# Kernel tuning notes

Hardware: AMD Instinct MI355X
Metric: run time of the kernel (lower is better)

The kernel has to match this reference:

```python
import jax, jax.numpy as jnp
import numpy as np

B, T, IN = 4096, 64, 3
D, H, NB = 128, 4, 2
DH = D // H  # 32
EPS = 1e-5


def layer_norm(x, g, b):
    mu = x.mean(-1, keepdims=True)
    v = x.var(-1, keepdims=True)
    return (x - mu) / jnp.sqrt(v + EPS) * g + b


def group_norm(x, g, b):
    # headwise GroupNorm over the last dim split into H groups of DH
    xr = x.reshape(x.shape[:-1] + (H, DH))
    mu = xr.mean(-1, keepdims=True)
    v = xr.var(-1, keepdims=True)
    xn = ((xr - mu) / jnp.sqrt(v + EPS)).reshape(x.shape)
    return xn * g + b


def slstm(xg, R):
    # xg: [B,T,4,D] input-driven gate preactivations (i,f,z,o)
    # R : [4,H,DH,DH] block-diagonal (per-head) recurrent kernels per gate
    Bb = xg.shape[0]

    def step(carry, g):
        h, c, n, m = carry  # each [B,D]
        r = jnp.einsum('bhd,ghde->bghe', h.reshape(Bb, H, DH), R).reshape(Bb, 4, D)
        g = g + r
        it, ft, zt, ot = g[:, 0], g[:, 1], g[:, 2], g[:, 3]
        m_new = jnp.maximum(ft + m, it)          # stabilizer state
        i = jnp.exp(it - m_new)                  # stabilized exp input gate
        f = jnp.exp(ft + m - m_new)              # stabilized exp forget gate
        c_new = f * c + i * jnp.tanh(zt)
        n_new = f * n + i                        # normalizer state
        h_new = jax.nn.sigmoid(ot) * c_new / n_new
        return (h_new, c_new, n_new, m_new), h_new

    init = tuple(jnp.zeros((Bb, D), xg.dtype) for _ in range(4))
    _, hs = jax.lax.scan(step, init, jnp.swapaxes(xg, 0, 1))  # [T,B,D]
    return jnp.swapaxes(hs, 0, 1)


def setup_inputs() -> dict:
    key = jax.random.key(0)
    ks = jax.random.split(key, 12)
    s_in = 1.0 / np.sqrt(IN)
    s_d = 1.0 / np.sqrt(D)
    inp = {
        'x': jax.random.normal(ks[0], (B, T, IN), jnp.float32),
        'w_in': jax.random.normal(ks[1], (IN, D), jnp.float32) * s_in,
        'b_in': jnp.zeros((D,), jnp.float32),
        'ln1_g': jnp.ones((NB, D), jnp.float32),
        'ln1_b': jnp.zeros((NB, D), jnp.float32),
        'Wg': jax.random.normal(ks[2], (NB, D, 4 * D), jnp.float32) * s_d,
        'bg': jnp.zeros((NB, 4 * D), jnp.float32),
        'Rg': jax.random.normal(ks[3], (NB, 4, H, DH, DH), jnp.float32) / np.sqrt(DH),
        'gn_g': jnp.ones((NB, D), jnp.float32),
        'gn_b': jnp.zeros((NB, D), jnp.float32),
        'ln2_g': jnp.ones((NB, D), jnp.float32),
        'ln2_b': jnp.zeros((NB, D), jnp.float32),
        'W1': jax.random.normal(ks[4], (NB, D, D), jnp.float32) * s_d,
        'W2': jax.random.normal(ks[5], (NB, D, D), jnp.float32) * s_d,
        'lnf_g': jnp.ones((D,), jnp.float32),
        'lnf_b': jnp.zeros((D,), jnp.float32),
        'w_out': jax.random.normal(ks[6], (D, 1), jnp.float32) * s_d,
        'b_out': jnp.zeros((1,), jnp.float32),
    }
    return inp


def reference(x, w_in, b_in, ln1_g, ln1_b, Wg, bg, Rg, gn_g, gn_b,
              ln2_g, ln2_b, W1, W2, lnf_g, lnf_b, w_out, b_out):
    h = x @ w_in + b_in  # [B,T,D]
    for blk in range(NB):
        # sLSTM sub-block (pre-LN residual)
        xn = layer_norm(h, ln1_g[blk], ln1_b[blk])
        xg = (xn @ Wg[blk] + bg[blk]).reshape(h.shape[0], T, 4, D)
        hs = slstm(xg, Rg[blk])
        h = h + group_norm(hs, gn_g[blk], gn_b[blk])
        # FFN sub-block (pre-LN residual, proj_factor=1.0, gelu, no bias)
        yn = layer_norm(h, ln2_g[blk], ln2_b[blk])
        h = h + jax.nn.gelu(yn @ W1[blk]) @ W2[blk]
    h = layer_norm(h, lnf_g, lnf_b)  # post-blocks norm
    out = (h[:, -1, :] @ w_out + b_out)[:, 0]  # [B]
    return out
```

## Files before the change

### kernel.cpp

```cpp
#include <hip/hip_runtime.h>
#include <hip/hip_bf16.h>
#include <cstdint>
#include <cstddef>

#define EPS 1e-5f
#define BB 4096
#define TT 64
#define NBLK 2
#define MROWS (BB * TT)

typedef unsigned short ushort_t;
typedef __attribute__((ext_vector_type(8))) short short8;
typedef __attribute__((ext_vector_type(4))) float floatx4;

__device__ __forceinline__ ushort_t f2b(float f) {
    __hip_bfloat16 h = __float2bfloat16(f);
    return *reinterpret_cast<ushort_t*>(&h);
}
__device__ __forceinline__ float tanh_fast(float z) {
    return 1.f - 2.f / (__expf(2.f * z) + 1.f);
}
__device__ __forceinline__ void lds_barrier() {
    asm volatile("s_waitcnt lgkmcnt(0)\n\ts_barrier" ::: "memory");
}

template <int CTRL>
__device__ __forceinline__ float ror_add(float v) {
    int r = __builtin_amdgcn_update_dpp(
        0, __builtin_bit_cast(int, v), CTRL, 0xf, 0xf, false);
    return v + __builtin_bit_cast(float, r);
}
__device__ __forceinline__ float red16(float v) {
    v = ror_add<0x121>(v);
    v = ror_add<0x122>(v);
    v = ror_add<0x124>(v);
    v = ror_add<0x128>(v);
    return v;
}

__global__ __launch_bounds__(256) void k_cvtall(
    const float* __restrict__ Wg, const float* __restrict__ W1,
    const float* __restrict__ W2, ushort_t* __restrict__ Wgt,
    ushort_t* __restrict__ W1t, ushort_t* __restrict__ W2t) {
    int idx = blockIdx.x * 256 + threadIdx.x;
    if (idx < 2 * 512 * 128) {
        int blk = idx >> 16, r = idx & 65535;
        int n = r >> 7, k = r & 127;
        Wgt[idx] = f2b(Wg[(size_t)blk * 65536 + k * 512 + n]);
    } else if (idx < 2 * 512 * 128 + 2 * 128 * 128) {
        int i2 = idx - 2 * 512 * 128;
        int blk = i2 >> 14, r = i2 & 16383;
        int n = r >> 7, k = r & 127;
        W1t[i2] = f2b(W1[(size_t)blk * 16384 + k * 128 + n]);
    } else {
        int i2 = idx - (2 * 512 * 128 + 2 * 128 * 128);
        int blk = i2 >> 14, r = i2 & 16383;
        int n = r >> 7, k = r & 127;
        W2t[i2] = f2b(W2[(size_t)blk * 16384 + k * 128 + n]);
    }
}

template <bool EMBED, bool LASTONLY>
__global__ __launch_bounds__(512, 2) void k_gslstm(
    float* __restrict__ h, const float* __restrict__ x,
    const float* __restrict__ w_in, const float* __restrict__ b_in,
    const ushort_t* __restrict__ Wgt, const float* __restrict__ bg,
    const float* __restrict__ Rg,
    const float* __restrict__ ln1g, const float* __restrict__ ln1b,
    const float* __restrict__ gng, const float* __restrict__ gnb) {
    __shared__ float xg_ring[2][512][20];
    __shared__ float hin_ring[3][16][132];
    __shared__ ushort_t Afrag[2][16][136];
    __shared__ ushort_t tpose[4][16][40];

    const int tid = threadIdx.x;
    const int lane = tid & 63;
    const int wave = tid >> 6;
    const int q = lane >> 4;
    const int ml = lane & 15;
    const int b0 = blockIdx.x * 16;

    if (wave < 4) {
        const int p = wave;
        const int row = p * 4 + q;
        short8 WB[4][8];
#pragma unroll
        for (int ks = 0; ks < 4; ++ks)
#pragma unroll
            for (int s = 0; s < 8; ++s)
                WB[ks][s] = *(const short8*)(Wgt +
                    ((size_t)(p * 128 + s * 16 + ml) * 128 + ks * 32 + q * 8));
        float biasv[8];
#pragma unroll
        for (int s = 0; s < 8; ++s) biasv[s] = bg[p * 128 + s * 16 + ml];

        auto issue_in = [&](int tt, float4& A, float4& B) {
            const float4* hp =
                (const float4*)(h + ((size_t)(b0 + row) * TT + tt) * 128 + ml * 8);
            A = hp[0]; B = hp[1];
        };
        auto issue_x = [&](int tt, float& x0, float& x1, float& x2) {
            const float* xp = x + ((size_t)(b0 + row) * TT + tt) * 3;
            x0 = xp[0]; x1 = xp[1]; x2 = xp[2];
        };
        auto embed_v = [&](float x0, float x1, float x2, float* v) {
            float4 w00 = *(const float4*)(w_in + 0 * 128 + ml * 8);
            float4 w01 = *(const float4*)(w_in + 0 * 128 + ml * 8 + 4);
            float4 w10 = *(const float4*)(w_in + 1 * 128 + ml * 8);
            float4 w11 = *(const float4*)(w_in + 1 * 128 + ml * 8 + 4);
            float4 w20 = *(const float4*)(w_in + 2 * 128 + ml * 8);
            float4 w21 = *(const float4*)(w_in + 2 * 128 + ml * 8 + 4);
            float4 be0 = *(const float4*)(b_in + ml * 8);
            float4 be1 = *(const float4*)(b_in + ml * 8 + 4);
            const float w0[8] = {w00.x, w00.y, w00.z, w00.w, w01.x, w01.y, w01.z, w01.w};
            const float w1[8] = {w10.x, w10.y, w10.z, w10.w, w11.x, w11.y, w11.z, w11.w};
            const float w2[8] = {w20.x, w20.y, w20.z, w20.w, w21.x, w21.y, w21.z, w21.w};
            const float be[8] = {be0.x, be0.y, be0.z, be0.w, be1.x, be1.y, be1.z, be1.w};
#pragma unroll
            for (int j = 0; j < 8; ++j)
                v[j] = x0 * w0[j] + x1 * w1[j] + x2 * w2[j] + be[j];
        };
        auto ln_stage = [&](const float* v, int aslot, int rslot) {
            float s = 0.f, ss = 0.f;
#pragma unroll
            for (int j = 0; j < 8; ++j) { s += v[j]; ss += v[j] * v[j]; }
            s = red16(s);
            ss = red16(ss);
            float mu = s * (1.f / 128.f);
            float rstd = rsqrtf(ss * (1.f / 128.f) - mu * mu + EPS);
            float4 g0 = *(const float4*)(ln1g + ml * 8);
            float4 g1 = *(const float4*)(ln1g + ml * 8 + 4);
            float4 c0 = *(const float4*)(ln1b + ml * 8);
            float4 c1 = *(const float4*)(ln1b + ml * 8 + 4);
            const float gg[8] = {g0.x, g0.y, g0.z, g0.w, g1.x, g1.y, g1.z, g1.w};
            const float bbv[8] = {c0.x, c0.y, c0.z, c0.w, c1.x, c1.y, c1.z, c1.w};
            ushort_t pk[8];
#pragma unroll
            for (int j = 0; j < 8; ++j)
                pk[j] = f2b((v[j] - mu) * rstd * gg[j] + bbv[j]);
            *(short8*)&Afrag[aslot][row][ml * 8] = *(const short8*)pk;
            *(float4*)&hin_ring[rslot][row][ml * 8] = *(const float4*)v;
            *(float4*)&hin_ring[rslot][row][ml * 8 + 4] = *(const float4*)(v + 4);
        };
        auto gemm_stage = [&](int slot) {
            short8 af[4];
#pragma unroll
            for (int ks = 0; ks < 4; ++ks)
                af[ks] = *(const short8*)&Afrag[slot][ml][ks * 32 + q * 8];
            floatx4 acc[8];
#pragma unroll
            for (int s = 0; s < 8; ++s) {
                float b = biasv[s];
                acc[s] = (floatx4){b, b, b, b};
            }
#pragma unroll
            for (int ks = 0; ks < 4; ++ks)
#pragma unroll
                for (int s = 0; s < 8; ++s)
                    acc[s] = __builtin_amdgcn_mfma_f32_16x16x32_bf16(
                        af[ks], WB[ks][s], acc[s], 0, 0, 0);
#pragma unroll
            for (int s = 0; s < 8; ++s)
                *(floatx4*)&xg_ring[slot][p * 128 + s * 16 + ml][q * 4] = acc[s];
        };

        float4 pA0, pA1, pB0, pB1;
        float px0 = 0.f, px1 = 0.f, px2 = 0.f, qx0 = 0.f, qx1 = 0.f, qx2 = 0.f;
        {
            float v[8];
            if (EMBED) {
                float a0, a1, a2, d0, d1, d2v;
                issue_x(0, a0, a1, a2);
                issue_x(1, d0, d1, d2v);
                issue_x(2, px0, px1, px2);
                embed_v(a0, a1, a2, v);  ln_stage(v, 0, 0);
                embed_v(d0, d1, d2v, v); ln_stage(v, 1, 1);
            } else {
                float4 a0, a1, d0, d1;
                issue_in(0, a0, a1);
                issue_in(1, d0, d1);
                issue_in(2, pA0, pA1);
                *(float4*)v = a0; *(float4*)(v + 4) = a1; ln_stage(v, 0, 0);
                *(float4*)v = d0; *(float4*)(v + 4) = d1; ln_stage(v, 1, 1);
            }
        }
        lds_barrier();
        gemm_stage(0);
        lds_barrier();

        int rs2 = 2, rs3 = 0;
#pragma unroll 1
        for (int t = 0; t < TT; t += 2) {
            if (t + 3 < TT) {
                if (EMBED) issue_x(t + 3, qx0, qx1, qx2);
                else       issue_in(t + 3, pB0, pB1);
            }
            gemm_stage((t + 1) & 1);
            if (t + 2 < TT) {
                float v[8];
                if (EMBED) embed_v(px0, px1, px2, v);
                else { *(float4*)v = pA0; *(float4*)(v + 4) = pA1; }
                ln_stage(v, t & 1, rs2);
            }
            lds_barrier();
            if (t + 4 < TT) {
                if (EMBED) issue_x(t + 4, px0, px1, px2);
                else       issue_in(t + 4, pA0, pA1);
            }
            if (t + 2 < TT) gemm_stage(t & 1);
            if (t + 3 < TT) {
                float v[8];
                if (EMBED) embed_v(qx0, qx1, qx2, v);
                else { *(float4*)v = pB0; *(float4*)(v + 4) = pB1; }
                ln_stage(v, (t + 1) & 1, rs3);
            }
            lds_barrier();
            rs2 += 2; if (rs2 >= 3) rs2 -= 3;
            rs3 += 2; if (rs3 >= 3) rs3 -= 3;
        }
    } else {
        __builtin_amdgcn_s_setprio(1);
        const int hd = wave - 4;
        short8 RB[4][2];
#pragma unroll
        for (int g = 0; g < 4; ++g)
#pragma unroll
            for (int d2 = 0; d2 < 2; ++d2) {
                ushort_t tmp[8];
#pragma unroll
                for (int j = 0; j < 8; ++j)
                    tmp[j] = f2b(Rg[(size_t)g * 4096 + hd * 1024 +
                                    (q * 8 + j) * 32 + d2 * 16 + ml]);
                RB[g][d2] = *(const short8*)tmp;
            }
        const float gng0 = gng[hd * 32 + ml], gng1 = gng[hd * 32 + 16 + ml];
        const float gnb0 = gnb[hd * 32 + ml], gnb1 = gnb[hd * 32 + 16 + ml];
        float cst[8], nst[8], mst[8];
#pragma unroll
        for (int i = 0; i < 8; ++i) { cst[i] = 0.f; nst[i] = 0.f; mst[i] = 0.f; }
        short8 h8 = {0, 0, 0, 0, 0, 0, 0, 0};

        auto scan_iter = [&](int t, int rs) {
            floatx4 acc[4][2];
#pragma unroll
            for (int g = 0; g < 4; ++g)
#pragma unroll
                for (int d2 = 0; d2 < 2; ++d2)
                    acc[g][d2] = *(const floatx4*)
                        &xg_ring[t & 1][g * 128 + hd * 32 + d2 * 16 + ml][q * 4];
#pragma unroll
            for (int g = 0; g < 4; ++g)
#pragma unroll
                for (int d2 = 0; d2 < 2; ++d2)
                    acc[g][d2] = __builtin_amdgcn_mfma_f32_16x16x32_bf16(
                        h8, RB[g][d2], acc[g][d2], 0, 0, 0);
            float hv[2][4];
#pragma unroll
            for (int d2 = 0; d2 < 2; ++d2)
#pragma unroll
                for (int r = 0; r < 4; ++r) {
                    const int si = d2 * 4 + r;
                    float it = acc[0][d2][r], ft = acc[1][d2][r];
                    float zt = acc[2][d2][r], ot = acc[3][d2][r];
                    float mn = fmaxf(ft + mst[si], it);
                    float iv = __expf(it - mn);
                    float fv = __expf(ft + mst[si] - mn);
                    float cn = fv * cst[si] + iv * tanh_fast(zt);
                    float nn = fv * nst[si] + iv;
                    hv[d2][r] = cn / (nn * (1.f + __expf(-ot)));
                    cst[si] = cn; nst[si] = nn; mst[si] = mn;
                }
#pragma unroll
            for (int d2 = 0; d2 < 2; ++d2)
#pragma unroll
                for (int r = 0; r < 4; ++r)
                    tpose[hd][q * 4 + r][d2 * 16 + ml] = f2b(hv[d2][r]);
            asm volatile("s_waitcnt lgkmcnt(0)" ::: "memory");
            h8 = *(const short8*)&tpose[hd][ml][q * 8];
            if (!LASTONLY || t == TT - 1) {
                float s[4], ss[4];
#pragma unroll
                for (int r = 0; r < 4; ++r) {
                    s[r] = hv[0][r] + hv[1][r];
                    ss[r] = hv[0][r] * hv[0][r] + hv[1][r] * hv[1][r];
                }
#pragma unroll
                for (int r = 0; r < 4; ++r) {
                    s[r] = red16(s[r]);
                    ss[r] = red16(ss[r]);
                }
#pragma unroll
                for (int r = 0; r < 4; ++r) {
                    float mu = s[r] * (1.f / 32.f);
                    float rstd = rsqrtf(ss[r] * (1.f / 32.f) - mu * mu + EPS);
#pragma unroll
                    for (int d2 = 0; d2 < 2; ++d2) {
                        float hin = hin_ring[rs][q * 4 + r][hd * 32 + d2 * 16 + ml];
                        float gv = d2 ? gng1 : gng0;
                        float bv = d2 ? gnb1 : gnb0;
                        h[((size_t)(b0 + q * 4 + r) * TT + t) * 128 +
                          hd * 32 + d2 * 16 + ml] =
                            hin + (hv[d2][r] - mu) * rstd * gv + bv;
                    }
                }
            }
        };

        lds_barrier();
        lds_barrier();
        int rs = 0;
#pragma unroll 1
        for (int t = 0; t < TT; t += 2) {
            scan_iter(t, rs);
            lds_barrier();
            scan_iter(t + 1, rs == 2 ? 0 : rs + 1);
            lds_barrier();
            rs += 2; if (rs >= 3) rs -= 3;
        }
    }
}

template <int NT>
__global__ __launch_bounds__(256, 4) void k_ffn_pipe(
    float* __restrict__ h, const ushort_t* __restrict__ W1t,
    const ushort_t* __restrict__ W2t,
    const float* __restrict__ lng, const float* __restrict__ lnb) {
    __shared__ ushort_t As[32][136];
    __shared__ ushort_t T1[32][136];
    __shared__ float T2[32][132];
    int tid = threadIdx.x;
    int lane = tid & 63, wave = tid >> 6;
    int q = lane >> 4, ml = lane & 15;
    int wn = wave * 32;
    int r = tid >> 3, qd = tid & 7;
    size_t base = (size_t)blockIdx.x * (32 * NT);

    short8 W1B[2][4];
#pragma unroll
    for (int jn = 0; jn < 2; ++jn)
#pragma unroll
        for (int ks = 0; ks < 4; ++ks)
            W1B[jn][ks] = *(const short8*)(W1t +
                ((size_t)(wn + jn * 16 + ml) * 128 + ks * 32 + q * 8));

    float4 cur[4], nxt[4];
    {
        const float4* hrow = (const float4*)(h + (base + r) * 128 + qd * 16);
#pragma unroll
        for (int k = 0; k < 4; ++k) cur[k] = hrow[k];
    }

#pragma unroll 1
    for (int it = 0; it < NT; ++it) {
        if (it + 1 < NT) {
            const float4* hrow =
                (const float4*)(h + (base + (it + 1) * 32 + r) * 128 + qd * 16);
#pragma unroll
            for (int k = 0; k < 4; ++k) nxt[k] = hrow[k];
        }
        float s = 0.f, ss = 0.f;
#pragma unroll
        for (int k = 0; k < 4; ++k) {
            float4 v = cur[k];
            s += v.x + v.y + v.z + v.w;
            ss += v.x * v.x + v.y * v.y + v.z * v.z + v.w * v.w;
        }
        s += __shfl_xor(s, 1); ss += __shfl_xor(ss, 1);
        s += __shfl_xor(s, 2); ss += __shfl_xor(ss, 2);
        s += __shfl_xor(s, 4); ss += __shfl_xor(ss, 4);
        float mu = s * (1.f / 128.f);
        float rstd = rsqrtf(ss * (1.f / 128.f) - mu * mu + EPS);
#pragma unroll
        for (int kk = 0; kk < 2; ++kk) {
            float4 a = cur[2 * kk];
            float4 b = cur[2 * kk + 1];
            int c0 = qd * 16 + kk * 8;
            float4 g0 = *(const float4*)(lng + c0);
            float4 g1 = *(const float4*)(lng + c0 + 4);
            float4 b0 = *(const float4*)(lnb + c0);
            float4 b1 = *(const float4*)(lnb + c0 + 4);
            ushort_t p[8];
            p[0] = f2b((a.x - mu) * rstd * g0.x + b0.x);
            p[1] = f2b((a.y - mu) * rstd * g0.y + b0.y);
            p[2] = f2b((a.z - mu) * rstd * g0.z + b0.z);
            p[3] = f2b((a.w - mu) * rstd * g0.w + b0.w);
            p[4] = f2b((b.x - mu) * rstd * g1.x + b1.x);
            p[5] = f2b((b.y - mu) * rstd * g1.y + b1.y);
            p[6] = f2b((b.z - mu) * rstd * g1.z + b1.z);
            p[7] = f2b((b.w - mu) * rstd * g1.w + b1.w);
            *(short8*)&As[r][c0] = *(const short8*)p;
        }
        lds_barrier();

        floatx4 acc[2][2];
#pragma unroll
        for (int i = 0; i < 2; ++i)
#pragma unroll
            for (int j = 0; j < 2; ++j) acc[i][j] = (floatx4)0.f;
#pragma unroll
        for (int ks = 0; ks < 4; ++ks) {
            short8 af[2];
#pragma unroll
            for (int im = 0; im < 2; ++im)
                af[im] = *(const short8*)&As[im * 16 + ml][ks * 32 + q * 8];
#pragma unroll
            for (int im = 0; im < 2; ++im)
#pragma unroll
                for (int jn = 0; jn < 2; ++jn)
                    acc[im][jn] = __builtin_amdgcn_mfma_f32_16x16x32_bf16(
                        af[im], W1B[jn][ks], acc[im][jn], 0, 0, 0);
        }
#pragma unroll
        for (int im = 0; im < 2; ++im)
#pragma unroll
            for (int jn = 0; jn < 2; ++jn)
#pragma unroll
                for (int rr = 0; rr < 4; ++rr) {
                    float v = acc[im][jn][rr];
                    float u = 0.7978845608028654f * (v + 0.044715f * v * v * v);
                    float gv = 0.5f * v * (1.f + tanh_fast(u));
                    T1[im * 16 + q * 4 + rr][wn + jn * 16 + ml] = f2b(gv);
                }
        short8 W2B[2][4];
#pragma unroll
        for (int jn = 0; jn < 2; ++jn)
#pragma unroll
            for (int ks = 0; ks < 4; ++ks)
                W2B[jn][ks] = *(const short8*)(W2t +
                    ((size_t)(wn + jn * 16 + ml) * 128 + ks * 32 + q * 8));
        lds_barrier();

#pragma unroll
        for (int i = 0; i < 2; ++i)
#pragma unroll
            for (int j = 0; j < 2; ++j) acc[i][j] = (floatx4)0.f;
#pragma unroll
        for (int ks = 0; ks < 4; ++ks) {
            short8 af[2];
#pragma unroll
            for (int im = 0; im < 2; ++im)
                af[im] = *(const short8*)&T1[im * 16 + ml][ks * 32 + q * 8];
#pragma unroll
            for (int im = 0; im < 2; ++im)
#pragma unroll
                for (int jn = 0; jn < 2; ++jn)
                    acc[im][jn] = __builtin_amdgcn_mfma_f32_16x16x32_bf16(
                        af[im], W2B[jn][ks], acc[im][jn], 0, 0, 0);
        }
#pragma unroll
        for (int im = 0; im < 2; ++im)
#pragma unroll
            for (int jn = 0; jn < 2; ++jn)
#pragma unroll
                for (int rr = 0; rr < 4; ++rr)
                    T2[im * 16 + q * 4 + rr][wn + jn * 16 + ml] = acc[im][jn][rr];
        lds_barrier();

        {
            float* hw = h + (base + it * 32 + r) * 128 + qd * 16;
#pragma unroll
            for (int k = 0; k < 4; ++k) {
                float4 t2v = *(const float4*)&T2[r][qd * 16 + k * 4];
                float4 o;
                o.x = cur[k].x + t2v.x;
                o.y = cur[k].y + t2v.y;
                o.z = cur[k].z + t2v.z;
                o.w = cur[k].w + t2v.w;
                ((float4*)hw)[k] = o;
            }
        }
#pragma unroll
        for (int k = 0; k < 4; ++k) cur[k] = nxt[k];
        lds_barrier();
    }
}

template <bool LAST>
__global__ __launch_bounds__(256, 6) void k_ffn(
    float* __restrict__ h, const ushort_t* __restrict__ W1t,
    const ushort_t* __restrict__ W2t,
    const float* __restrict__ lng, const float* __restrict__ lnb) {
    __shared__ ushort_t As[32][136];
    __shared__ ushort_t T1[32][136];
    int tid = threadIdx.x;
    int lane = tid & 63, wave = tid >> 6;
    int q = lane >> 4, ml = lane & 15;
    int wn = wave * 32;
    size_t row0 = (size_t)blockIdx.x * 32;

    short8 W1B[2][4];
#pragma unroll
    for (int jn = 0; jn < 2; ++jn)
#pragma unroll
        for (int ks = 0; ks < 4; ++ks)
            W1B[jn][ks] = *(const short8*)(W1t +
                ((size_t)(wn + jn * 16 + ml) * 128 + ks * 32 + q * 8));

    int r = tid >> 3, qd = tid & 7;
    size_t grow = LAST ? ((row0 + r) * TT + (TT - 1)) : (row0 + r);
    const float* hrow = h + grow * 128 + qd * 16;
    float s = 0.f, ss = 0.f;
#pragma unroll
    for (int k = 0; k < 4; ++k) {
        float4 v = ((const float4*)hrow)[k];
        s += v.x + v.y + v.z + v.w;
        ss += v.x * v.x + v.y * v.y + v.z * v.z + v.w * v.w;
    }
    s += __shfl_xor(s, 1); ss += __shfl_xor(ss, 1);
    s += __shfl_xor(s, 2); ss += __shfl_xor(ss, 2);
    s += __shfl_xor(s, 4); ss += __shfl_xor(ss, 4);
    float mu = s * (1.f / 128.f);
    float rstd = rsqrtf(ss * (1.f / 128.f) - mu * mu + EPS);
#pragma unroll
    for (int kk = 0; kk < 2; ++kk) {
        float4 a = ((const float4*)hrow)[2 * kk];
        float4 b = ((const float4*)hrow)[2 * kk + 1];
        int c0 = qd * 16 + kk * 8;
        float4 g0 = *(const float4*)(lng + c0);
        float4 g1 = *(const float4*)(lng + c0 + 4);
        float4 b0 = *(const float4*)(lnb + c0);
        float4 b1 = *(const float4*)(lnb + c0 + 4);
        ushort_t p[8];
        p[0] = f2b((a.x - mu) * rstd * g0.x + b0.x);
        p[1] = f2b((a.y - mu) * rstd * g0.y + b0.y);
        p[2] = f2b((a.z - mu) * rstd * g0.z + b0.z);
        p[3] = f2b((a.w - mu) * rstd * g0.w + b0.w);
        p[4] = f2b((b.x - mu) * rstd * g1.x + b1.x);
        p[5] = f2b((b.y - mu) * rstd * g1.y + b1.y);
        p[6] = f2b((b.z - mu) * rstd * g1.z + b1.z);
        p[7] = f2b((b.w - mu) * rstd * g1.w + b1.w);
        *(short8*)&As[r][c0] = *(const short8*)p;
    }
    lds_barrier();

    floatx4 acc[2][2];
#pragma unroll
    for (int i = 0; i < 2; ++i)
#pragma unroll
        for (int j = 0; j < 2; ++j) acc[i][j] = (floatx4)0.f;
#pragma unroll
    for (int ks = 0; ks < 4; ++ks) {
        short8 af[2];
#pragma unroll
        for (int im = 0; im < 2; ++im)
            af[im] = *(const short8*)&As[im * 16 + ml][ks * 32 + q * 8];
#pragma unroll
        for (int im = 0; im < 2; ++im)
#pragma unroll
            for (int jn = 0; jn < 2; ++jn)
                acc[im][jn] = __builtin_amdgcn_mfma_f32_16x16x32_bf16(
                    af[im], W1B[jn][ks], acc[im][jn], 0, 0, 0);
    }
#pragma unroll
    for (int im = 0; im < 2; ++im)
#pragma unroll
        for (int jn = 0; jn < 2; ++jn)
#pragma unroll
            for (int rr = 0; rr < 4; ++rr) {
                float v = acc[im][jn][rr];
                float u = 0.7978845608028654f * (v + 0.044715f * v * v * v);
                float gv = 0.5f * v * (1.f + tanh_fast(u));
                T1[im * 16 + q * 4 + rr][wn + jn * 16 + ml] = f2b(gv);
            }
    short8 W2B[2][4];
#pragma unroll
    for (int jn = 0; jn < 2; ++jn)
#pragma unroll
        for (int ks = 0; ks < 4; ++ks)
            W2B[jn][ks] = *(const short8*)(W2t +
                ((size_t)(wn + jn * 16 + ml) * 128 + ks * 32 + q * 8));
    lds_barrier();

#pragma unroll
    for (int i = 0; i < 2; ++i)
#pragma unroll
        for (int j = 0; j < 2; ++j) acc[i][j] = (floatx4)0.f;
#pragma unroll
    for (int ks = 0; ks < 4; ++ks) {
        short8 af[2];
#pragma unroll
        for (int im = 0; im < 2; ++im)
            af[im] = *(const short8*)&T1[im * 16 + ml][ks * 32 + q * 8];
#pragma unroll
        for (int im = 0; im < 2; ++im)
#pragma unroll
            for (int jn = 0; jn < 2; ++jn)
                acc[im][jn] = __builtin_amdgcn_mfma_f32_16x16x32_bf16(
                    af[im], W2B[jn][ks], acc[im][jn], 0, 0, 0);
    }
#pragma unroll
    for (int im = 0; im < 2; ++im)
#pragma unroll
        for (int jn = 0; jn < 2; ++jn)
#pragma unroll
            for (int rr = 0; rr < 4; ++rr) {
                int rloc = im * 16 + q * 4 + rr;
                size_t rw = LAST ? ((row0 + rloc) * TT + (TT - 1)) : (row0 + rloc);
                int cc = wn + jn * 16 + ml;
                h[rw * 128 + cc] += acc[im][jn][rr];
            }
}

__global__ __launch_bounds__(256) void k_out(const float* __restrict__ h,
                                             const float* __restrict__ lnfg,
                                             const float* __restrict__ lnfb,
                                             const float* __restrict__ w_out,
                                             const float* __restrict__ b_out,
                                             float* __restrict__ out) {
    int b = blockIdx.x * 4 + (threadIdx.x >> 6);
    int l = threadIdx.x & 63;
    const float* hr = h + ((size_t)b * TT + (TT - 1)) * 128;
    float2 v = *(const float2*)(hr + l * 2);
    float s = v.x + v.y, ss = v.x * v.x + v.y * v.y;
#pragma unroll
    for (int off = 1; off < 64; off <<= 1) {
        s += __shfl_xor(s, off);
        ss += __shfl_xor(ss, off);
    }
    float mu_ = s * (1.f / 128.f);
    float rstd = rsqrtf(ss * (1.f / 128.f) - mu_ * mu_ + EPS);
    float2 g = *(const float2*)(lnfg + l * 2);
    float2 bb = *(const float2*)(lnfb + l * 2);
    float2 w = *(const float2*)(w_out + l * 2);
    float dot = ((v.x - mu_) * rstd * g.x + bb.x) * w.x +
                ((v.y - mu_) * rstd * g.y + bb.y) * w.y;
#pragma unroll
    for (int off = 1; off < 64; off <<= 1) dot += __shfl_xor(dot, off);
    if (l == 0) out[b] = dot + b_out[0];
}

extern "C" void kernel_launch(void* const* d_in, const int* in_sizes, int n_in,
                              void* d_out, int out_size, void* d_ws, size_t ws_size,
                              hipStream_t stream) {
    const float* x    = (const float*)d_in[0];
    const float* w_in = (const float*)d_in[1];
    const float* b_in = (const float*)d_in[2];
    const float* ln1g = (const float*)d_in[3];
    const float* ln1b = (const float*)d_in[4];
    const float* Wg   = (const float*)d_in[5];
    const float* bg   = (const float*)d_in[6];
    const float* Rg   = (const float*)d_in[7];
    const float* gng  = (const float*)d_in[8];
    const float* gnb  = (const float*)d_in[9];
    const float* ln2g = (const float*)d_in[10];
    const float* ln2b = (const float*)d_in[11];
    const float* W1   = (const float*)d_in[12];
    const float* W2   = (const float*)d_in[13];
    const float* lnfg = (const float*)d_in[14];
    const float* lnfb = (const float*)d_in[15];
    const float* wout = (const float*)d_in[16];
    const float* bout = (const float*)d_in[17];
    float* out = (float*)d_out;

    float* h = (float*)d_ws;
    ushort_t* Wgt = (ushort_t*)(h + (size_t)MROWS * 128);
    ushort_t* W1t = Wgt + 2 * 512 * 128;
    ushort_t* W2t = W1t + 2 * 128 * 128;

    k_cvtall<<<(2 * 512 * 128 + 4 * 128 * 128) / 256, 256, 0, stream>>>(
        Wg, W1, W2, Wgt, W1t, W2t);

    k_gslstm<true, false><<<BB / 16, 512, 0, stream>>>(
        h, x, w_in, b_in, Wgt, bg, Rg, ln1g, ln1b, gng, gnb);
    k_ffn_pipe<8><<<MROWS / 256, 256, 0, stream>>>(h, W1t, W2t, ln2g, ln2b);
    k_gslstm<false, true><<<BB / 16, 512, 0, stream>>>(
        h, nullptr, nullptr, nullptr, Wgt + (size_t)512 * 128, bg + 512,
        Rg + (size_t)16384, ln1g + 128, ln1b + 128, gng + 128, gnb + 128);
    k_ffn<true><<<BB / 32, 256, 0, stream>>>(h, W1t + 16384, W2t + 16384,
                                             ln2g + 128, ln2b + 128);
    k_out<<<BB / 4, 256, 0, stream>>>(h, lnfg, lnfb, wout, bout, out);
}
```

Measured before the change: 403.9 us.

## Coalesce FFN global loads/stores via LDS staging and double tiles per block

```diff
diff --git a/kernel.cpp b/kernel.cpp
--- a/kernel.cpp
+++ b/kernel.cpp
@@ -321,18 +321,22 @@
 }
 
 template <int NT>
-__global__ __launch_bounds__(256, 4) void k_ffn_pipe(
+__global__ __launch_bounds__(256, 2) void k_ffn_pipe(
     float* __restrict__ h, const ushort_t* __restrict__ W1t,
     const ushort_t* __restrict__ W2t,
     const float* __restrict__ lng, const float* __restrict__ lnb) {
-    __shared__ ushort_t As[32][136];
+    __shared__ float Hraw[32][132];
     __shared__ ushort_t T1[32][136];
-    __shared__ float T2[32][132];
+    __shared__ __align__(16) char Ubuf[32 * 132 * 4];
+    auto As = (ushort_t(*)[136])Ubuf;
+    auto T2 = (float(*)[132])Ubuf;
+
     int tid = threadIdx.x;
     int lane = tid & 63, wave = tid >> 6;
     int q = lane >> 4, ml = lane & 15;
     int wn = wave * 32;
     int r = tid >> 3, qd = tid & 7;
+    int hi = lane >> 5, lo = lane & 31;
     size_t base = (size_t)blockIdx.x * (32 * NT);
 
     short8 W1B[2][4];
@@ -344,24 +348,31 @@
                 ((size_t)(wn + jn * 16 + ml) * 128 + ks * 32 + q * 8));
 
     float4 cur[4], nxt[4];
-    {
-        const float4* hrow = (const float4*)(h + (base + r) * 128 + qd * 16);
-#pragma unroll
-        for (int k = 0; k < 4; ++k) cur[k] = hrow[k];
-    }
+#pragma unroll
+    for (int k = 0; k < 4; ++k)
+        cur[k] = *(const float4*)(h + (base + wave * 8 + 2 * k + hi) * 128 + lo * 4);
 
 #pragma unroll 1
     for (int it = 0; it < NT; ++it) {
+#pragma unroll
+        for (int k = 0; k < 4; ++k)
+            *(float4*)&Hraw[wave * 8 + 2 * k + hi][lo * 4] = cur[k];
         if (it + 1 < NT) {
-            const float4* hrow =
-                (const float4*)(h + (base + (it + 1) * 32 + r) * 128 + qd * 16);
-#pragma unroll
-            for (int k = 0; k < 4; ++k) nxt[k] = hrow[k];
-        }
+#pragma unroll
+            for (int k = 0; k < 4; ++k)
+                nxt[k] = *(const float4*)(h +
+                    (base + (it + 1) * 32 + wave * 8 + 2 * k + hi) * 128 + lo * 4);
+        }
+        lds_barrier();
+
+        float4 hv[4];
+#pragma unroll
+        for (int k = 0; k < 4; ++k)
+            hv[k] = *(const float4*)&Hraw[r][qd * 16 + k * 4];
         float s = 0.f, ss = 0.f;
 #pragma unroll
         for (int k = 0; k < 4; ++k) {
-            float4 v = cur[k];
+            float4 v = hv[k];
             s += v.x + v.y + v.z + v.w;
             ss += v.x * v.x + v.y * v.y + v.z * v.z + v.w * v.w;
         }
@@ -372,8 +383,8 @@
         float rstd = rsqrtf(ss * (1.f / 128.f) - mu * mu + EPS);
 #pragma unroll
         for (int kk = 0; kk < 2; ++kk) {
-            float4 a = cur[2 * kk];
-            float4 b = cur[2 * kk + 1];
+            float4 a = hv[2 * kk];
+            float4 b = hv[2 * kk + 1];
             int c0 = qd * 16 + kk * 8;
             float4 g0 = *(const float4*)(lng + c0);
             float4 g1 = *(const float4*)(lng + c0 + 4);
@@ -456,21 +467,20 @@
                     T2[im * 16 + q * 4 + rr][wn + jn * 16 + ml] = acc[im][jn][rr];
         lds_barrier();
 
-        {
-            float* hw = h + (base + it * 32 + r) * 128 + qd * 16;
-#pragma unroll
-            for (int k = 0; k < 4; ++k) {
-                float4 t2v = *(const float4*)&T2[r][qd * 16 + k * 4];
-                float4 o;
-                o.x = cur[k].x + t2v.x;
-                o.y = cur[k].y + t2v.y;
-                o.z = cur[k].z + t2v.z;
-                o.w = cur[k].w + t2v.w;
-                ((float4*)hw)[k] = o;
-            }
-        }
-#pragma unroll
-        for (int k = 0; k < 4; ++k) cur[k] = nxt[k];
+#pragma unroll
+        for (int k = 0; k < 4; ++k) {
+            float4 t2v = *(const float4*)&T2[wave * 8 + 2 * k + hi][lo * 4];
+            float4 o;
+            o.x = cur[k].x + t2v.x;
+            o.y = cur[k].y + t2v.y;
+            o.z = cur[k].z + t2v.z;
+            o.w = cur[k].w + t2v.w;
+            *(float4*)(h + (base + it * 32 + wave * 8 + 2 * k + hi) * 128 + lo * 4) = o;
+        }
+        if (it + 1 < NT) {
+#pragma unroll
+            for (int k = 0; k < 4; ++k) cur[k] = nxt[k];
+        }
         lds_barrier();
     }
 }
@@ -662,7 +672,7 @@
 
     k_gslstm<true, false><<<BB / 16, 512, 0, stream>>>(
         h, x, w_in, b_in, Wgt, bg, Rg, ln1g, ln1b, gng, gnb);
-    k_ffn_pipe<8><<<MROWS / 256, 256, 0, stream>>>(h, W1t, W2t, ln2g, ln2b);
+    k_ffn_pipe<16><<<MROWS / 512, 256, 0, stream>>>(h, W1t, W2t, ln2g, ln2b);
     k_gslstm<false, true><<<BB / 16, 512, 0, stream>>>(
         h, nullptr, nullptr, nullptr, Wgt + (size_t)512 * 128, bg + 512,
         Rg + (size_t)16384, ln1g + 128, ln1b + 128, gng + 128, gnb + 128);
```

Result: faster. 357.5 us (-11.5%).
